# Performance work log

Measured on AMD Instinct MI355X. Metric: run time of the kernel, lower is better.

## Reference

```python
import jax, jax.numpy as jnp
import numpy as np

B_, N_, D_ = 8, 1024, 64
H_, DH_ = 4, 16
DI_, DS_, DTR_ = 128, 64, 4
MAXP = 512


def _ln(x, w, b, eps=1e-5):
    m = jnp.mean(x, -1, keepdims=True)
    v = jnp.mean((x - m) ** 2, -1, keepdims=True)
    return (x - m) * jax.lax.rsqrt(v + eps) * w + b


def _attn(x, drop_mask, Wq, Wkv, Wo, bo, rel_emb):
    b, n, d = x.shape
    scale = DH_ ** -0.5
    q = (x @ Wq).reshape(b, n, H_, DH_).transpose(0, 2, 1, 3)
    kv = x @ Wkv
    k = kv[..., :d].reshape(b, n, H_, DH_).transpose(0, 2, 1, 3)
    v = kv[..., d:].reshape(b, n, H_, DH_).transpose(0, 2, 1, 3)
    dots = jnp.einsum('bhid,bhjd->bhij', q, k) * scale
    seq = jnp.arange(n)
    dist = jnp.clip(seq[:, None] - seq[None, :], -MAXP, MAXP) + MAXP
    rpe = rel_emb[dist]  # (n, n, DH_)
    dots = dots + jnp.einsum('bhid,ijd->bhij', q, rpe) * scale
    # stochastic key drop: Bernoulli(0.3) positions get -1e12
    dots = dots + drop_mask.astype(dots.dtype) * (-1e12)
    attn = jax.nn.softmax(dots, axis=-1)
    out = jnp.einsum('bhij,bhjd->bhid', attn, v)
    out = out.transpose(0, 2, 1, 3).reshape(b, n, H_ * DH_)
    return out @ Wo + bo


def _mamba(x, W_in, conv_w, conv_b, W_xproj, W_dt, b_dt, A_log, Dm, W_out):
    b, n, _ = x.shape
    xz = x @ W_in                      # (b, n, 2*DI_)
    u, z = xz[..., :DI_], xz[..., DI_:]
    uc = u.transpose(0, 2, 1)          # (b, DI_, n)
    uc = jax.lax.conv_general_dilated(
        uc, conv_w[:, None, :], (1,), ((3, 0),),
        feature_group_count=DI_, dimension_numbers=('NCH', 'OIH', 'NCH'))
    uc = uc + conv_b[None, :, None]
    u = jax.nn.silu(uc).transpose(0, 2, 1)  # (b, n, DI_)
    xdb = u @ W_xproj                  # (b, n, DTR_+2*DS_)
    dt = jax.nn.softplus(xdb[..., :DTR_] @ W_dt + b_dt)  # (b, n, DI_)
    Bm = xdb[..., DTR_:DTR_ + DS_]
    Cm = xdb[..., DTR_ + DS_:]
    A = -jnp.exp(A_log)                # (DI_, DS_)

    def step(h, inp):
        dt_t, B_t, C_t, u_t = inp      # (b,DI_),(b,DS_),(b,DS_),(b,DI_)
        dA = jnp.exp(dt_t[..., None] * A)
        h = h * dA + (dt_t * u_t)[..., None] * B_t[:, None, :]
        y = jnp.einsum('bds,bs->bd', h, C_t)
        return h, y

    h0 = jnp.zeros((b, DI_, DS_), x.dtype)
    xs = (dt.transpose(1, 0, 2), Bm.transpose(1, 0, 2),
          Cm.transpose(1, 0, 2), u.transpose(1, 0, 2))
    _, ys = jax.lax.scan(step, h0, xs)
    y = ys.transpose(1, 0, 2) + u * Dm
    y = y * jax.nn.silu(z)
    return y @ W_out


def _rmsgn(x, gamma, eps=1e-5, groups=4):
    shp = x.shape
    dpg = shp[-1] // groups
    xg = x.reshape(shp[:-1] + (groups, dpg))
    rms = jnp.sqrt(jnp.sum(xg * xg, -1, keepdims=True)) * (dpg ** -0.5)
    return (xg / (rms + eps)).reshape(shp) * gamma


def _ff1(x, c1_w, c1_b, d1_w, d1_b):
    # SwiGLUConvDeconv1d(64, 256, kernel=4, shift=1); x: (b, s2, 64)
    s2 = x.shape[1]
    xc = x.transpose(0, 2, 1)
    xc = jnp.pad(xc, ((0, 0), (0, 0), (3, 3)))
    xc = jax.lax.conv_general_dilated(
        xc, c1_w, (1,), 'VALID', dimension_numbers=('NCH', 'OIH', 'NCH'))
    xc = xc + c1_b[None, :, None]
    gate = jax.nn.silu(xc[:, 256:, :])
    xc = xc[:, :256, :] * gate
    # ConvTranspose1d stride 1 == conv with flipped kernel, full padding
    w = jnp.flip(d1_w, -1).transpose(1, 0, 2)  # (64, 256, 4)
    xc = jax.lax.conv_general_dilated(
        xc, w, (1,), ((3, 3),), dimension_numbers=('NCH', 'OIH', 'NCH'))
    xc = xc + d1_b[None, :, None]
    out = xc.transpose(0, 2, 1)
    return out[:, 3:3 + s2, :]


def _forward(x, drop_mask, ln1_w, ln1_b, Wq, Wkv, Wo, bo, rel_emb,
             ln2_w, ln2_b, W_in, conv_w, conv_b, W_xproj, W_dt, b_dt,
             A_log, Dm, W_out, gamma, c1_w, c1_b, d1_w, d1_b, ln3_w, ln3_b):
    xt = _ln(x, ln1_w, ln1_b)
    xt = _attn(xt, drop_mask, Wq, Wkv, Wo, bo, rel_emb) + x
    x = x + xt  # dropout p=0 -> identity (faithful to original residual math)
    xt = _ln(x, ln2_w, ln2_b)
    m = _mamba(xt, W_in, conv_w, conv_b, W_xproj, W_dt, b_dt, A_log, Dm, W_out)
    m = jnp.where(m >= 0, m, 0.01 * m)  # leaky_relu
    m = _rmsgn(m, gamma)
    m = m + 0.5 * _ff1(m, c1_w, c1_b, d1_w, d1_b)
    x = x + m
    return _ln(x, ln3_w, ln3_b)


def setup_inputs() -> dict:
    ks = jax.random.split(jax.random.key(0), 16)
    g = lambda i, shp, s: jax.random.normal(ks[i], shp, dtype=jnp.float32) * s
    A_log = jnp.log(jnp.tile(jnp.arange(1, DS_ + 1, dtype=jnp.float32)[None, :], (DI_, 1)))
    return {
        'x': jax.random.normal(ks[0], (B_, N_, D_), dtype=jnp.float32),
        'drop_mask': jax.random.bernoulli(ks[1], 0.3, (B_, H_, N_, N_)),
        'ln1_w': jnp.ones((D_,), jnp.float32), 'ln1_b': jnp.zeros((D_,), jnp.float32),
        'Wq': g(2, (D_, D_), 0.1), 'Wkv': g(3, (D_, 2 * D_), 0.1),
        'Wo': g(4, (D_, D_), 0.1), 'bo': jnp.zeros((D_,), jnp.float32),
        'rel_emb': g(5, (2 * MAXP + 1, DH_), 0.02),
        'ln2_w': jnp.ones((D_,), jnp.float32), 'ln2_b': jnp.zeros((D_,), jnp.float32),
        'W_in': g(6, (D_, 2 * DI_), 0.1),
        'conv_w': g(7, (DI_, 4), 0.2), 'conv_b': jnp.zeros((DI_,), jnp.float32),
        'W_xproj': g(8, (DI_, DTR_ + 2 * DS_), 0.1),
        'W_dt': g(9, (DTR_, DI_), 0.1), 'b_dt': jnp.zeros((DI_,), jnp.float32),
        'A_log': A_log, 'Dm': jnp.ones((DI_,), jnp.float32),
        'W_out': g(10, (DI_, D_), 0.1),
        'gamma': jnp.ones((D_,), jnp.float32),
        'c1_w': g(11, (512, 64, 4), 0.1), 'c1_b': jnp.zeros((512,), jnp.float32),
        'd1_w': g(12, (256, 64, 4), 0.1), 'd1_b': jnp.zeros((64,), jnp.float32),
        'ln3_w': jnp.ones((D_,), jnp.float32), 'ln3_b': jnp.zeros((D_,), jnp.float32),
    }


def reference(x, drop_mask, ln1_w, ln1_b, Wq, Wkv, Wo, bo, rel_emb,
              ln2_w, ln2_b, W_in, conv_w, conv_b, W_xproj, W_dt, b_dt,
              A_log, Dm, W_out, gamma, c1_w, c1_b, d1_w, d1_b, ln3_w, ln3_b):
    return _forward(x, drop_mask, ln1_w, ln1_b, Wq, Wkv, Wo, bo, rel_emb,
                    ln2_w, ln2_b, W_in, conv_w, conv_b, W_xproj, W_dt, b_dt,
                    A_log, Dm, W_out, gamma, c1_w, c1_b, d1_w, d1_b, ln3_w, ln3_b)
```

## Files before the change

### kernel.cpp

```cpp
#include <hip/hip_runtime.h>
#include <math.h>


__device__ __forceinline__ float wsum64(float v){
#pragma unroll
  for(int m=32;m>0;m>>=1) v += __shfl_xor(v, m, 64);
  return v;
}
__device__ __forceinline__ float wmax64(float v){
#pragma unroll
  for(int m=32;m>0;m>>=1) v = fmaxf(v, __shfl_xor(v, m, 64));
  return v;
}
__device__ __forceinline__ float silu_f(float x){ return x / (1.f + __expf(-x)); }
__device__ __forceinline__ int clip512(int d){ return d < -512 ? -512 : (d > 512 ? 512 : d); }

__global__ __launch_bounds__(256) void k_ln1_qkv(
    const float* __restrict__ x, const float* __restrict__ w1, const float* __restrict__ b1,
    const float* __restrict__ Wq, const float* __restrict__ Wkv,
    const float* __restrict__ rel, const float* __restrict__ c1w,
    float* __restrict__ qb, float2* __restrict__ kvT,
    float* __restrict__ relT, float* __restrict__ c1wT){
  int lane = threadIdx.x & 63, warp = threadIdx.x >> 6;
  int token = blockIdx.x*4 + warp;
  __shared__ float xt[4][64];
  float xv = x[(size_t)token*64 + lane];
  float mean = wsum64(xv) * 0.015625f;
  float dlt = xv - mean;
  float var = wsum64(dlt*dlt) * 0.015625f;
  float xn = dlt * rsqrtf(var + 1e-5f) * w1[lane] + b1[lane];
  xt[warp][lane] = xn;
  __syncthreads();
  float aq=0.f, ak=0.f, av=0.f;
#pragma unroll 4
  for(int dd=0; dd<64; ++dd){
    float xd = xt[warp][dd];
    aq += xd * Wq[dd*64 + lane];
    ak += xd * Wkv[dd*128 + lane];
    av += xd * Wkv[dd*128 + 64 + lane];
  }
  int b = token >> 10, i = token & 1023;
  int h = lane >> 4, dh = lane & 15;
  size_t o  = (((size_t)(b*4 + h))*1024 + i)*16 + dh;
  size_t oT = (((size_t)(b*4 + h))*16 + dh)*1024 + i;
  qb[o]=aq;
  kvT[oT] = make_float2(ak, av);

  if (blockIdx.x < 65){
    int idx = blockIdx.x*256 + threadIdx.x;
    if (idx < 16*1025){
      int c = idx / 1025;
      int d = idx - c*1025;
      relT[idx] = rel[d*16 + c];
    }
  } else if (blockIdx.x < 577){
    int idx = (blockIdx.x-65)*256 + threadIdx.x;
    int row = idx >> 9;
    int ii  = idx & 511;
    c1wT[idx] = c1w[(size_t)ii*256 + row];
  }
}

__global__ __launch_bounds__(256, 3) void k_attn(
    const float* __restrict__ qb, const float2* __restrict__ kvT,
    const int* __restrict__ dmask, const float* __restrict__ relT,
    float* __restrict__ attn_raw){
  int tid = threadIdx.x;
  int lane = tid & 63, wv = tid >> 6;
  int bh  = blockIdx.y;
  int i0  = blockIdx.x*8;
  int b = bh >> 2, h = bh & 3;
  int r0 = wv*2, r1 = wv*2 + 1;
  int i_a = i0 + r0, i_b = i0 + r1;

  __shared__ float Gc[8][1024];
  __shared__ float qs[8][16];
  __shared__ float sums[8];

  if (tid < 128){
    int r = tid >> 4, c = tid & 15;
    qs[r][c] = qb[((size_t)bh*1024 + i0 + r)*16 + c] * 0.25f;
  }
  __syncthreads();

  {
    int r = tid >> 5, jb = tid & 31;
#pragma unroll 1
    for(int k=0;k<32;++k){
      int j = jb + 32*k;
      int d = clip512(i0 + r - j) + 512;
      float g = 0.f;
#pragma unroll
      for(int c=0;c<16;++c) g += qs[r][c]*relT[c*1025 + d];
      Gc[r][j] = g;
    }
  }
  float q0[16], q1[16];
#pragma unroll
  for(int c=0;c<16;++c){ q0[c]=qs[r0][c]; q1[c]=qs[r1][c]; }
  __syncthreads();

  const float2* kvb = kvT + (size_t)bh*16*1024;
  const int* mb0 = dmask + ((size_t)bh*1024 + i_a)*1024;
  const int* mb1 = dmask + ((size_t)bh*1024 + i_b)*1024;

  float m0=-3.0e38f, m1=-3.0e38f, s0=0.f, s1=0.f;
  float a0[16], a1[16];
#pragma unroll
  for(int c=0;c<16;++c){ a0[c]=0.f; a1[c]=0.f; }

#pragma unroll 1
  for(int t=0;t<16;++t){
    int j = lane + 64*t;
    int mk0 = mb0[j], mk1 = mb1[j];
    float2 kv[16];
#pragma unroll
    for(int c=0;c<16;++c) kv[c] = kvb[c*1024 + j];
    float sv0 = Gc[r0][j] + (mk0 ? -1.0e12f : 0.0f);
    float sv1 = Gc[r1][j] + (mk1 ? -1.0e12f : 0.0f);
#pragma unroll
    for(int c=0;c<16;++c){ sv0 += q0[c]*kv[c].x; sv1 += q1[c]*kv[c].x; }
    float mn0 = fmaxf(m0, sv0);
    float al0 = __expf(m0 - mn0);
    float p0  = __expf(sv0 - mn0);
    m0 = mn0; s0 = s0*al0 + p0;
#pragma unroll
    for(int c=0;c<16;++c) a0[c] = a0[c]*al0 + p0*kv[c].y;
    float mn1 = fmaxf(m1, sv1);
    float al1 = __expf(m1 - mn1);
    float p1  = __expf(sv1 - mn1);
    m1 = mn1; s1 = s1*al1 + p1;
#pragma unroll
    for(int c=0;c<16;++c) a1[c] = a1[c]*al1 + p1*kv[c].y;
  }
  float M0 = wmax64(m0), M1 = wmax64(m1);
  float sc0 = __expf(m0 - M0), sc1 = __expf(m1 - M1);
  s0 = wsum64(s0*sc0); s1 = wsum64(s1*sc1);
#pragma unroll
  for(int c=0;c<16;++c){
    float x0 = a0[c]*sc0;
    x0 += __shfl_xor(x0, 32, 64); x0 += __shfl_xor(x0, 16, 64);
    a0[c] = x0;
    float x1 = a1[c]*sc1;
    x1 += __shfl_xor(x1, 32, 64); x1 += __shfl_xor(x1, 16, 64);
    a1[c] = x1;
  }
  __syncthreads();
  float* red = &Gc[0][0];
  if (lane < 16){
#pragma unroll
    for(int c=0;c<16;++c){
      red[r0*272 + lane*17 + c] = a0[c];
      red[r1*272 + lane*17 + c] = a1[c];
    }
  }
  if (lane == 0){ sums[r0] = s0; sums[r1] = s1; }
  __syncthreads();
  if (tid < 128){
    int row = tid >> 4, c = tid & 15;
    float tot = 0.f;
#pragma unroll
    for(int g=0; g<16; ++g) tot += red[row*272 + g*17 + c];
    int irow = i0 + row;
    attn_raw[((size_t)b*1024 + irow)*64 + h*16 + c] = tot / sums[row];
  }
}

__global__ __launch_bounds__(256) void k_post_attn(
    const float* __restrict__ x, const float* __restrict__ attn_raw,
    const float* __restrict__ Wo, const float* __restrict__ bo,
    const float* __restrict__ ln2w, const float* __restrict__ ln2b,
    const float* __restrict__ W_in,
    float* __restrict__ x2, float* __restrict__ u0, float* __restrict__ zsarr){
  int lane = threadIdx.x & 63, warp = threadIdx.x >> 6;
  int token = blockIdx.x*4 + warp;
  __shared__ float ar[4][64];
  __shared__ float lnv[4][64];
  ar[warp][lane] = attn_raw[(size_t)token*64 + lane];
  __syncthreads();
  float acc = bo[lane];
#pragma unroll 4
  for(int dd=0;dd<64;++dd) acc += ar[warp][dd]*Wo[dd*64+lane];
  float t = 2.f*x[(size_t)token*64+lane] + acc;
  x2[(size_t)token*64+lane] = t;
  float mean = wsum64(t)*0.015625f;
  float dlt = t-mean;
  float var = wsum64(dlt*dlt)*0.015625f;
  float ln = dlt*rsqrtf(var+1e-5f)*ln2w[lane]+ln2b[lane];
  lnv[warp][lane]=ln;
  __syncthreads();
  float a0=0.f,a1=0.f,a2=0.f,a3=0.f;
#pragma unroll 4
  for(int dd=0;dd<64;++dd){
    float xd = lnv[warp][dd];
    const float* wr = W_in + dd*256;
    a0 += xd*wr[lane]; a1 += xd*wr[lane+64]; a2 += xd*wr[lane+128]; a3 += xd*wr[lane+192];
  }
  u0[(size_t)token*128 + lane] = a0;
  u0[(size_t)token*128 + 64 + lane] = a1;
  zsarr[(size_t)token*128 + lane] = silu_f(a2);
  zsarr[(size_t)token*128 + 64 + lane] = silu_f(a3);
}

__global__ __launch_bounds__(256) void k_conv_proj(
    const float* __restrict__ u0, const float* __restrict__ conv_w, const float* __restrict__ conv_b,
    const float* __restrict__ W_xproj, const float* __restrict__ W_dt, const float* __restrict__ b_dt,
    float* __restrict__ uarr, float* __restrict__ Bmp, float* __restrict__ Cmp, float* __restrict__ dtarr){
  int sub = threadIdx.x >> 7, c = threadIdx.x & 127;
  int token = blockIdx.x*2 + sub;
  int b = token >> 10, i = token & 1023;
  __shared__ float us[2][128];
  __shared__ float dtin[2][4];
  float acc = conv_b[c];
#pragma unroll
  for(int k2=0;k2<4;++k2){
    int t2 = i - 3 + k2;
    if (t2 >= 0) acc += u0[((size_t)b*1024 + t2)*128 + c]*conv_w[c*4+k2];
  }
  float uv = silu_f(acc);
  uarr[(size_t)token*128 + c] = uv;
  us[sub][c] = uv;
  __syncthreads();
  float accA = 0.f, accB = 0.f;
  int cB = 128 + (c & 3);
#pragma unroll 4
  for(int dd=0; dd<128; ++dd){
    float xd = us[sub][dd];
    accA += xd * W_xproj[dd*132 + c];
    accB += xd * W_xproj[dd*132 + cB];
  }
  if (c < 4){ dtin[sub][c] = accA; Cmp[(size_t)token*64 + 60 + c] = accB; }
  else if (c < 68) Bmp[(size_t)token*64 + (c-4)] = accA;
  else             Cmp[(size_t)token*64 + (c-68)] = accA;
  __syncthreads();
  float dv = b_dt[c];
#pragma unroll
  for(int r2=0;r2<4;++r2) dv += dtin[sub][r2]*W_dt[r2*128 + c];
  dv = fmaxf(dv, 0.f) + log1pf(expf(-fabsf(dv)));
  dtarr[(size_t)token*128 + c] = dv;
}

__global__ __launch_bounds__(256) void k_scan(
    const float* __restrict__ dtarr, const float* __restrict__ uarr,
    const float* __restrict__ Bmp, const float* __restrict__ Cmp,
    const float* __restrict__ zsarr, const float* __restrict__ A_log,
    const float* __restrict__ Dm, float* __restrict__ ymp){
  int lane = threadIdx.x & 63, warp = threadIdx.x >> 6;
  int g = blockIdx.x*4 + warp;
  int b = g >> 7, d = g & 127;
  float A = -expf(A_log[d*64 + lane]);
  float Dv = Dm[d];
  const float* dtp = dtarr + (size_t)b*1024*128 + d;
  const float* up  = uarr  + (size_t)b*1024*128 + d;
  const float* zp  = zsarr + (size_t)b*1024*128 + d;
  const float* Bp  = Bmp   + (size_t)b*1024*64 + lane;
  const float* Cp  = Cmp   + (size_t)b*1024*64 + lane;
  float* yp        = ymp   + (size_t)b*1024*128 + d;
  float h = 0.f;
  for(int t0=0; t0<1024; t0+=8){
    float dtc[8], uc[8], Bc[8], Cc[8], zc[8];
#pragma unroll
    for(int r=0;r<8;++r){
      dtc[r]=dtp[(size_t)(t0+r)*128]; uc[r]=up[(size_t)(t0+r)*128];
      Bc[r]=Bp[(size_t)(t0+r)*64];    Cc[r]=Cp[(size_t)(t0+r)*64];
      zc[r]=zp[(size_t)(t0+r)*128];
    }
    float hc[8];
#pragma unroll
    for(int r=0;r<8;++r){
      float dt = dtc[r];
      h = h*__expf(dt*A) + dt*uc[r]*Bc[r];
      hc[r] = h*Cc[r];
    }
    float y[8];
#pragma unroll
    for(int r=0;r<8;++r) y[r] = wsum64(hc[r]);
    if (lane==0){
#pragma unroll
      for(int r=0;r<8;++r) yp[(size_t)(t0+r)*128] = (y[r] + uc[r]*Dv)*zc[r];
    }
  }
}

__global__ __launch_bounds__(256) void k_wout(
    const float* __restrict__ ymp, const float* __restrict__ W_out,
    const float* __restrict__ gamma, float* __restrict__ marr){
  int lane = threadIdx.x & 63, warp = threadIdx.x >> 6;
  int token = blockIdx.x*4 + warp;
  __shared__ float ys[4][128];
  ys[warp][lane]      = ymp[(size_t)token*128 + lane];
  ys[warp][lane+64]   = ymp[(size_t)token*128 + 64 + lane];
  __syncthreads();
  float acc = 0.f;
#pragma unroll 4
  for(int dd=0; dd<128; ++dd) acc += ys[warp][dd]*W_out[dd*64 + lane];
  acc = acc >= 0.f ? acc : 0.01f*acc;
  float ss = acc*acc;
#pragma unroll
  for(int m=1;m<16;m<<=1) ss += __shfl_xor(ss, m, 64);
  float rms = sqrtf(ss)*0.25f;
  marr[(size_t)token*64 + lane] = acc/(rms + 1e-5f)*gamma[lane];
}

__global__ __launch_bounds__(256) void k_h2(
    const float* __restrict__ marr, const float* __restrict__ c1wT,
    const float* __restrict__ c1b, float* __restrict__ h2){
  int b = blockIdx.y;
  int t0 = blockIdx.x * 16;
  int tid = threadIdx.x;
  __shared__ float ms[19][64];
  for(int l = tid; l < 19*64; l += 256){
    int row = l >> 6, cc = l & 63;
    int t = t0 - 3 + row;
    ms[row][cc] = (t >= 0 && t < 1024) ? marr[((size_t)b*1024 + t)*64 + cc] : 0.f;
  }
  __syncthreads();
  int i = tid;
  float acc1[16], acc2[16];
#pragma unroll
  for(int tl=0;tl<16;++tl){ acc1[tl]=0.f; acc2[tl]=0.f; }
  for(int cc=0; cc<64; ++cc){
    float mv[19];
#pragma unroll
    for(int r2=0;r2<19;++r2) mv[r2] = ms[r2][cc];
    const float* wr = c1wT + (size_t)cc*4*512;
    float wa0 = wr[      i], wa1 = wr[ 512+i], wa2 = wr[1024+i], wa3 = wr[1536+i];
    float wg0 = wr[  256+i], wg1 = wr[ 768+i], wg2 = wr[1280+i], wg3 = wr[1792+i];
#pragma unroll
    for(int tl=0; tl<16; ++tl){
      acc1[tl] += wa0*mv[tl+0] + wa1*mv[tl+1] + wa2*mv[tl+2] + wa3*mv[tl+3];
      acc2[tl] += wg0*mv[tl+0] + wg1*mv[tl+1] + wg2*mv[tl+2] + wg3*mv[tl+3];
    }
  }
  float bb1 = c1b[i], bb2 = c1b[i+256];
#pragma unroll
  for(int tl=0; tl<16; ++tl){
    int t = t0 + tl;
    if (t < 1027){
      float o1 = acc1[tl] + bb1;
      float o2 = acc2[tl] + bb2;
      h2[((size_t)b*1027 + t)*256 + i] = o1 * silu_f(o2);
    }
  }
}

__global__ __launch_bounds__(256) void k_ff_final(
    const float* __restrict__ h2, const float* __restrict__ d1w, const float* __restrict__ d1b,
    const float* __restrict__ x2, const float* __restrict__ marr,
    const float* __restrict__ ln3w, const float* __restrict__ ln3b,
    float* __restrict__ out){
  int b = blockIdx.y;
  int s0 = blockIdx.x * 16;
  int tid = threadIdx.x;
  int o = tid & 63, sg = tid >> 6;
  __shared__ float hs[19][256];
  for(int l = tid; l < 19*256; l += 256){
    int row = l >> 8, cc = l & 255;
    hs[row][cc] = h2[((size_t)b*1027 + s0 + row)*256 + cc];
  }
  __syncthreads();
  int sl = sg*4;
  float acc0=0.f, acc1=0.f, acc2=0.f, acc3=0.f;
  const float4* wb = (const float4*)d1w + o;
#pragma unroll 2
  for(int i2=0; i2<256; ++i2){
    float4 wv = wb[(size_t)i2*64];
    float h0=hs[sl+0][i2], h1=hs[sl+1][i2], h2v=hs[sl+2][i2], h3=hs[sl+3][i2];
    float h4=hs[sl+4][i2], h5=hs[sl+5][i2], h6=hs[sl+6][i2];
    acc0 += h0*wv.w + h1*wv.z + h2v*wv.y + h3*wv.x;
    acc1 += h1*wv.w + h2v*wv.z + h3*wv.y + h4*wv.x;
    acc2 += h2v*wv.w + h3*wv.z + h4*wv.y + h5*wv.x;
    acc3 += h3*wv.w + h4*wv.z + h5*wv.y + h6*wv.x;
  }
  float accs[4] = {acc0, acc1, acc2, acc3};
  float bo_ = d1b[o];
#pragma unroll
  for(int r=0;r<4;++r){
    int s = s0 + sl + r;
    size_t idx = ((size_t)b*1024 + s)*64 + o;
    float tot = x2[idx] + marr[idx] + 0.5f*(accs[r] + bo_);
    float mean = wsum64(tot)*0.015625f;
    float dlt = tot - mean;
    float var = wsum64(dlt*dlt)*0.015625f;
    out[idx] = dlt*rsqrtf(var+1e-5f)*ln3w[o] + ln3b[o];
  }
}

extern "C" void kernel_launch(void* const* d_in, const int* in_sizes, int n_in,
                              void* d_out, int out_size, void* d_ws, size_t ws_size,
                              hipStream_t stream){
  const float* x       = (const float*)d_in[0];
  const int*   dmask   = (const int*)  d_in[1];
  const float* ln1w    = (const float*)d_in[2];
  const float* ln1b    = (const float*)d_in[3];
  const float* Wq      = (const float*)d_in[4];
  const float* Wkv     = (const float*)d_in[5];
  const float* Wo      = (const float*)d_in[6];
  const float* bo      = (const float*)d_in[7];
  const float* rel     = (const float*)d_in[8];
  const float* ln2w    = (const float*)d_in[9];
  const float* ln2b    = (const float*)d_in[10];
  const float* W_in    = (const float*)d_in[11];
  const float* conv_w  = (const float*)d_in[12];
  const float* conv_b  = (const float*)d_in[13];
  const float* W_xproj = (const float*)d_in[14];
  const float* W_dt    = (const float*)d_in[15];
  const float* b_dt    = (const float*)d_in[16];
  const float* A_log   = (const float*)d_in[17];
  const float* Dm      = (const float*)d_in[18];
  const float* W_out   = (const float*)d_in[19];
  const float* gamma   = (const float*)d_in[20];
  const float* c1w     = (const float*)d_in[21];
  const float* c1b     = (const float*)d_in[22];
  const float* d1w     = (const float*)d_in[23];
  const float* d1b     = (const float*)d_in[24];
  const float* ln3w    = (const float*)d_in[25];
  const float* ln3b    = (const float*)d_in[26];
  float* outp = (float*)d_out;

  float* ws = (float*)d_ws;
  float* qb       = ws;
  float* kvT      = qb      + 524288;
  float* attn_raw = kvT     + 1048576;
  float* x2       = attn_raw+ 524288;
  float* u0       = x2      + 524288;
  float* zsarr    = u0      + 1048576;
  float* uarr     = zsarr   + 1048576;
  float* dtarr    = uarr    + 1048576;
  float* Bmp      = dtarr   + 1048576;
  float* Cmp      = Bmp     + 524288;
  float* ymp      = Cmp     + 524288;
  float* marr     = ymp     + 1048576;
  float* h2       = marr    + 524288;
  float* relT     = h2      + 2103296;
  float* c1wT     = relT    + 16400;

  k_ln1_qkv  <<<2048, 256, 0, stream>>>(x, ln1w, ln1b, Wq, Wkv, rel, c1w,
                                        qb, (float2*)kvT, relT, c1wT);
  k_attn     <<<dim3(128,32), 256, 0, stream>>>(qb, (const float2*)kvT, dmask, relT, attn_raw);
  k_post_attn<<<2048, 256, 0, stream>>>(x, attn_raw, Wo, bo, ln2w, ln2b, W_in, x2, u0, zsarr);
  k_conv_proj<<<4096, 256, 0, stream>>>(u0, conv_w, conv_b, W_xproj, W_dt, b_dt, uarr, Bmp, Cmp, dtarr);
  k_scan     <<<256, 256, 0, stream>>>(dtarr, uarr, Bmp, Cmp, zsarr, A_log, Dm, ymp);
  k_wout     <<<2048, 256, 0, stream>>>(ymp, W_out, gamma, marr);
  k_h2       <<<dim3(65,8), 256, 0, stream>>>(marr, c1wT, c1b, h2);
  k_ff_final <<<dim3(64,8), 256, 0, stream>>>(h2, d1w, d1b, x2, marr, ln3w, ln3b, outp);
}
```

Measured before the change: 808.1 us.

## Chunk the Mamba scan, use a precomputed softmax bound, and pack KV as float4

The selective scan now splits the 1024-step recurrence into 8 chunks. A first kernel computes each chunk's decay product and partial state, and a second kernel combines the prefix and rescans its chunk, which raises parallelism from 256 to 2048 waves. Attention replaces the online softmax with a fixed upper bound per row: the max of the relative-position term plus |q|·max|k|, where max|k| comes from a new small kernel. Masked positions are skipped with a select instead of the -1e12 add. KV is stored interleaved so it loads as float4, and the attention occupancy hint goes from 3 to 4; the bound can underflow exp if it is loose, and the scan now reads dt, u and B twice.

Result: no change. 814.1 us (+0.7%).

```diff
diff --git a/kernel.cpp b/kernel.cpp
--- a/kernel.cpp
+++ b/kernel.cpp
@@ -19,7 +19,7 @@
     const float* __restrict__ x, const float* __restrict__ w1, const float* __restrict__ b1,
     const float* __restrict__ Wq, const float* __restrict__ Wkv,
     const float* __restrict__ rel, const float* __restrict__ c1w,
-    float* __restrict__ qb, float2* __restrict__ kvT,
+    float* __restrict__ qb, float2* __restrict__ kvT4,
     float* __restrict__ relT, float* __restrict__ c1wT){
   int lane = threadIdx.x & 63, warp = threadIdx.x >> 6;
   int token = blockIdx.x*4 + warp;
@@ -42,9 +42,10 @@
   int b = token >> 10, i = token & 1023;
   int h = lane >> 4, dh = lane & 15;
   size_t o  = (((size_t)(b*4 + h))*1024 + i)*16 + dh;
-  size_t oT = (((size_t)(b*4 + h))*16 + dh)*1024 + i;
   qb[o]=aq;
-  kvT[oT] = make_float2(ak, av);
+  int c2 = dh >> 1, half = dh & 1;
+  size_t o2 = ((((size_t)(b*4 + h))*8 + c2)*1024 + i)*2 + half;
+  kvT4[o2] = make_float2(ak, av);
 
   if (blockIdx.x < 65){
     int idx = blockIdx.x*256 + threadIdx.x;
@@ -61,20 +62,42 @@
   }
 }
 
-__global__ __launch_bounds__(256, 3) void k_attn(
-    const float* __restrict__ qb, const float2* __restrict__ kvT,
+__global__ __launch_bounds__(256) void k_kmax(
+    const float4* __restrict__ kvT4, float* __restrict__ Kmax){
+  int bh = blockIdx.x; int tid = threadIdx.x;
+  const float4* base = kvT4 + (size_t)bh*8*1024;
+  float mx = 0.f;
+#pragma unroll
+  for(int r=0;r<4;++r){
+    int j = tid + 256*r;
+    float ss = 0.f;
+#pragma unroll
+    for(int c2=0;c2<8;++c2){ float4 kv = base[c2*1024 + j]; ss += kv.x*kv.x + kv.z*kv.z; }
+    mx = fmaxf(mx, ss);
+  }
+  mx = wmax64(mx);
+  __shared__ float red[4];
+  int lane = tid&63, wv = tid>>6;
+  if(lane==0) red[wv]=mx;
+  __syncthreads();
+  if(tid==0) Kmax[bh] = sqrtf(fmaxf(fmaxf(red[0],red[1]),fmaxf(red[2],red[3])));
+}
+
+__global__ __launch_bounds__(256, 4) void k_attn(
+    const float* __restrict__ qb, const float4* __restrict__ kvT4,
     const int* __restrict__ dmask, const float* __restrict__ relT,
-    float* __restrict__ attn_raw){
+    const float* __restrict__ Kmax, float* __restrict__ attn_raw){
   int tid = threadIdx.x;
   int lane = tid & 63, wv = tid >> 6;
   int bh  = blockIdx.y;
   int i0  = blockIdx.x*8;
   int b = bh >> 2, h = bh & 3;
   int r0 = wv*2, r1 = wv*2 + 1;
-  int i_a = i0 + r0, i_b = i0 + r1;
 
   __shared__ float Gc[8][1024];
   __shared__ float qs[8][16];
+  __shared__ float gmS[8];
+  __shared__ float Ms[8];
   __shared__ float sums[8];
 
   if (tid < 128){
@@ -85,26 +108,43 @@
 
   {
     int r = tid >> 5, jb = tid & 31;
+    float qr[16];
+#pragma unroll
+    for(int c=0;c<16;++c) qr[c] = qs[r][c];
+    float gmax = -3.0e38f;
 #pragma unroll 1
     for(int k=0;k<32;++k){
       int j = jb + 32*k;
       int d = clip512(i0 + r - j) + 512;
       float g = 0.f;
 #pragma unroll
-      for(int c=0;c<16;++c) g += qs[r][c]*relT[c*1025 + d];
+      for(int c=0;c<16;++c) g += qr[c]*relT[c*1025 + d];
       Gc[r][j] = g;
-    }
-  }
+      gmax = fmaxf(gmax, g);
+    }
+#pragma unroll
+    for(int m=1;m<32;m<<=1) gmax = fmaxf(gmax, __shfl_xor(gmax, m, 64));
+    if ((lane&31)==0) gmS[r] = gmax;
+  }
+  __syncthreads();
+  if (tid < 8){
+    float qn = 0.f;
+#pragma unroll
+    for(int c=0;c<16;++c) qn += qs[tid][c]*qs[tid][c];
+    Ms[tid] = gmS[tid] + sqrtf(qn)*Kmax[bh];
+  }
+  __syncthreads();
+
   float q0[16], q1[16];
 #pragma unroll
   for(int c=0;c<16;++c){ q0[c]=qs[r0][c]; q1[c]=qs[r1][c]; }
-  __syncthreads();
-
-  const float2* kvb = kvT + (size_t)bh*16*1024;
-  const int* mb0 = dmask + ((size_t)bh*1024 + i_a)*1024;
-  const int* mb1 = dmask + ((size_t)bh*1024 + i_b)*1024;
-
-  float m0=-3.0e38f, m1=-3.0e38f, s0=0.f, s1=0.f;
+  float M0 = Ms[r0], M1 = Ms[r1];
+
+  const float4* kvb = kvT4 + (size_t)bh*8*1024;
+  const int* mb0 = dmask + ((size_t)bh*1024 + i0 + r0)*1024;
+  const int* mb1 = dmask + ((size_t)bh*1024 + i0 + r1)*1024;
+
+  float s0=0.f, s1=0.f;
   float a0[16], a1[16];
 #pragma unroll
   for(int c=0;c<16;++c){ a0[c]=0.f; a1[c]=0.f; }
@@ -113,35 +153,31 @@
   for(int t=0;t<16;++t){
     int j = lane + 64*t;
     int mk0 = mb0[j], mk1 = mb1[j];
-    float2 kv[16];
-#pragma unroll
-    for(int c=0;c<16;++c) kv[c] = kvb[c*1024 + j];
-    float sv0 = Gc[r0][j] + (mk0 ? -1.0e12f : 0.0f);
-    float sv1 = Gc[r1][j] + (mk1 ? -1.0e12f : 0.0f);
-#pragma unroll
-    for(int c=0;c<16;++c){ sv0 += q0[c]*kv[c].x; sv1 += q1[c]*kv[c].x; }
-    float mn0 = fmaxf(m0, sv0);
-    float al0 = __expf(m0 - mn0);
-    float p0  = __expf(sv0 - mn0);
-    m0 = mn0; s0 = s0*al0 + p0;
-#pragma unroll
-    for(int c=0;c<16;++c) a0[c] = a0[c]*al0 + p0*kv[c].y;
-    float mn1 = fmaxf(m1, sv1);
-    float al1 = __expf(m1 - mn1);
-    float p1  = __expf(sv1 - mn1);
-    m1 = mn1; s1 = s1*al1 + p1;
-#pragma unroll
-    for(int c=0;c<16;++c) a1[c] = a1[c]*al1 + p1*kv[c].y;
-  }
-  float M0 = wmax64(m0), M1 = wmax64(m1);
-  float sc0 = __expf(m0 - M0), sc1 = __expf(m1 - M1);
-  s0 = wsum64(s0*sc0); s1 = wsum64(s1*sc1);
+    float4 kv[8];
+#pragma unroll
+    for(int c2=0;c2<8;++c2) kv[c2] = kvb[c2*1024 + j];
+    float sv0 = Gc[r0][j], sv1 = Gc[r1][j];
+#pragma unroll
+    for(int c2=0;c2<8;++c2){
+      sv0 += q0[2*c2]*kv[c2].x + q0[2*c2+1]*kv[c2].z;
+      sv1 += q1[2*c2]*kv[c2].x + q1[2*c2+1]*kv[c2].z;
+    }
+    float p0 = mk0 ? 0.f : __expf(sv0 - M0);
+    float p1 = mk1 ? 0.f : __expf(sv1 - M1);
+    s0 += p0; s1 += p1;
+#pragma unroll
+    for(int c2=0;c2<8;++c2){
+      a0[2*c2]   += p0*kv[c2].y; a0[2*c2+1] += p0*kv[c2].w;
+      a1[2*c2]   += p1*kv[c2].y; a1[2*c2+1] += p1*kv[c2].w;
+    }
+  }
+  s0 = wsum64(s0); s1 = wsum64(s1);
 #pragma unroll
   for(int c=0;c<16;++c){
-    float x0 = a0[c]*sc0;
+    float x0 = a0[c];
     x0 += __shfl_xor(x0, 32, 64); x0 += __shfl_xor(x0, 16, 64);
     a0[c] = x0;
-    float x1 = a1[c]*sc1;
+    float x1 = a1[c];
     x1 += __shfl_xor(x1, 32, 64); x1 += __shfl_xor(x1, 16, 64);
     a1[c] = x1;
   }
@@ -161,8 +197,7 @@
     float tot = 0.f;
 #pragma unroll
     for(int g=0; g<16; ++g) tot += red[row*272 + g*17 + c];
-    int irow = i0 + row;
-    attn_raw[((size_t)b*1024 + irow)*64 + h*16 + c] = tot / sums[row];
+    attn_raw[((size_t)b*1024 + i0 + row)*64 + h*16 + c] = tot / sums[row];
   }
 }
 
@@ -240,24 +275,63 @@
   dtarr[(size_t)token*128 + c] = dv;
 }
 
-__global__ __launch_bounds__(256) void k_scan(
+__global__ __launch_bounds__(256) void k_scan_a(
+    const float* __restrict__ dtarr, const float* __restrict__ uarr,
+    const float* __restrict__ Bmp, const float* __restrict__ A_log,
+    float* __restrict__ Parr, float* __restrict__ Rarr){
+  int lane = threadIdx.x & 63, warp = threadIdx.x >> 6;
+  int w = blockIdx.x*4 + warp;
+  int c = w & 7, d = (w >> 3) & 127, b = w >> 10;
+  float A = -expf(A_log[d*64 + lane]);
+  int tb = c*128;
+  const float* dtp = dtarr + ((size_t)b*1024 + tb)*128 + d;
+  const float* up  = uarr  + ((size_t)b*1024 + tb)*128 + d;
+  const float* Bp  = Bmp   + ((size_t)b*1024 + tb)*64 + lane;
+  float R = 0.f, sdt = 0.f;
+  for(int t0=0; t0<128; t0+=8){
+    float dtc[8], uc[8], Bc[8];
+#pragma unroll
+    for(int r=0;r<8;++r){
+      dtc[r]=dtp[(size_t)(t0+r)*128]; uc[r]=up[(size_t)(t0+r)*128]; Bc[r]=Bp[(size_t)(t0+r)*64];
+    }
+#pragma unroll
+    for(int r=0;r<8;++r){
+      float dt = dtc[r];
+      R = R*__expf(dt*A) + dt*uc[r]*Bc[r];
+      sdt += dt;
+    }
+  }
+  Parr[(size_t)w*64 + lane] = __expf(sdt*A);
+  Rarr[(size_t)w*64 + lane] = R;
+}
+
+__global__ __launch_bounds__(256) void k_scan_c(
     const float* __restrict__ dtarr, const float* __restrict__ uarr,
     const float* __restrict__ Bmp, const float* __restrict__ Cmp,
     const float* __restrict__ zsarr, const float* __restrict__ A_log,
-    const float* __restrict__ Dm, float* __restrict__ ymp){
+    const float* __restrict__ Dm, const float* __restrict__ Parr,
+    const float* __restrict__ Rarr, float* __restrict__ ymp){
   int lane = threadIdx.x & 63, warp = threadIdx.x >> 6;
-  int g = blockIdx.x*4 + warp;
-  int b = g >> 7, d = g & 127;
+  int w = blockIdx.x*4 + warp;
+  int c = w & 7, d = (w >> 3) & 127, b = w >> 10;
   float A = -expf(A_log[d*64 + lane]);
   float Dv = Dm[d];
-  const float* dtp = dtarr + (size_t)b*1024*128 + d;
-  const float* up  = uarr  + (size_t)b*1024*128 + d;
-  const float* zp  = zsarr + (size_t)b*1024*128 + d;
-  const float* Bp  = Bmp   + (size_t)b*1024*64 + lane;
-  const float* Cp  = Cmp   + (size_t)b*1024*64 + lane;
-  float* yp        = ymp   + (size_t)b*1024*128 + d;
   float h = 0.f;
-  for(int t0=0; t0<1024; t0+=8){
+  int wbase = w - c;
+#pragma unroll 1
+  for(int cp=0; cp<c; ++cp){
+    float P = Parr[(size_t)(wbase+cp)*64 + lane];
+    float R = Rarr[(size_t)(wbase+cp)*64 + lane];
+    h = h*P + R;
+  }
+  int tb = c*128;
+  const float* dtp = dtarr + ((size_t)b*1024 + tb)*128 + d;
+  const float* up  = uarr  + ((size_t)b*1024 + tb)*128 + d;
+  const float* zp  = zsarr + ((size_t)b*1024 + tb)*128 + d;
+  const float* Bp  = Bmp   + ((size_t)b*1024 + tb)*64 + lane;
+  const float* Cp  = Cmp   + ((size_t)b*1024 + tb)*64 + lane;
+  float* yp        = ymp   + ((size_t)b*1024 + tb)*128 + d;
+  for(int t0=0; t0<128; t0+=8){
     float dtc[8], uc[8], Bc[8], Cc[8], zc[8];
 #pragma unroll
     for(int r=0;r<8;++r){
@@ -420,8 +494,8 @@
 
   float* ws = (float*)d_ws;
   float* qb       = ws;
-  float* kvT      = qb      + 524288;
-  float* attn_raw = kvT     + 1048576;
+  float* kvT4     = qb      + 524288;
+  float* attn_raw = kvT4    + 1048576;
   float* x2       = attn_raw+ 524288;
   float* u0       = x2      + 524288;
   float* zsarr    = u0      + 1048576;
@@ -434,13 +508,18 @@
   float* h2       = marr    + 524288;
   float* relT     = h2      + 2103296;
   float* c1wT     = relT    + 16400;
+  float* Parr     = c1wT    + 131072;
+  float* Rarr     = Parr    + 524288;
+  float* Kmaxa    = Rarr    + 524288;
 
   k_ln1_qkv  <<<2048, 256, 0, stream>>>(x, ln1w, ln1b, Wq, Wkv, rel, c1w,
-                                        qb, (float2*)kvT, relT, c1wT);
-  k_attn     <<<dim3(128,32), 256, 0, stream>>>(qb, (const float2*)kvT, dmask, relT, attn_raw);
+                                        qb, (float2*)kvT4, relT, c1wT);
+  k_kmax     <<<32, 256, 0, stream>>>((const float4*)kvT4, Kmaxa);
+  k_attn     <<<dim3(128,32), 256, 0, stream>>>(qb, (const float4*)kvT4, dmask, relT, Kmaxa, attn_raw);
   k_post_attn<<<2048, 256, 0, stream>>>(x, attn_raw, Wo, bo, ln2w, ln2b, W_in, x2, u0, zsarr);
   k_conv_proj<<<4096, 256, 0, stream>>>(u0, conv_w, conv_b, W_xproj, W_dt, b_dt, uarr, Bmp, Cmp, dtarr);
-  k_scan     <<<256, 256, 0, stream>>>(dtarr, uarr, Bmp, Cmp, zsarr, A_log, Dm, ymp);
+  k_scan_a   <<<2048, 256, 0, stream>>>(dtarr, uarr, Bmp, A_log, Parr, Rarr);
+  k_scan_c   <<<2048, 256, 0, stream>>>(dtarr, uarr, Bmp, Cmp, zsarr, A_log, Dm, Parr, Rarr, ymp);
   k_wout     <<<2048, 256, 0, stream>>>(ymp, W_out, gamma, marr);
   k_h2       <<<dim3(65,8), 256, 0, stream>>>(marr, c1wT, c1b, h2);
   k_ff_final <<<dim3(64,8), 256, 0, stream>>>(h2, d1w, d1b, x2, marr, ln3w, ln3b, outp);
```
